# Optimization experiments

Hardware: AMD Instinct MI355X
Metric: run time of the kernel (lower is better)

## Reference

```python
import jax, jax.numpy as jnp
import numpy as np

N = 8192      # batch*seq_len (batch=4, seq_len=2048)
DK = 256
DV = 256


def setup_inputs() -> dict:
    key = jax.random.key(0)
    ks = jax.random.split(key, 9)
    s = 1.0 / np.sqrt(DK)
    return {
        "q": jax.random.normal(ks[0], (N, DK), jnp.float32),
        "k": jax.random.normal(ks[1], (N, DK), jnp.float32),
        "v": jax.random.normal(ks[2], (N, DV), jnp.float32),
        "Wq": jax.random.normal(ks[3], (DK, DK), jnp.float32) * s,
        "bq": jnp.zeros((DK,), jnp.float32),
        "Wk": jax.random.normal(ks[4], (DK, DK), jnp.float32) * s,
        "bk": jnp.zeros((DK,), jnp.float32),
        "Wv": jax.random.normal(ks[5], (DV, DV), jnp.float32) * s,
        "bv": jnp.zeros((DV,), jnp.float32),
        "seq_len": 2048,
    }


def reference(q, k, v, Wq, bq, Wk, bk, Wv, bv, seq_len):
    # torch Linear: y = x @ W.T + b
    Q = q @ Wq.T + bq                       # [N, dk]
    K = k @ Wk.T + bk                       # [N, dk]
    V = v @ Wv.T + bv                       # [N, dv]
    sqrt_dk = jnp.sqrt(jnp.asarray(DK, Q.dtype))
    score = (Q @ K.T) / sqrt_dk             # [N, N] — attends over ALL tokens
    # original reshapes to (B, S, N) and softmaxes over dim=-1, which is
    # identical to row-wise softmax on the [N, N] score matrix
    attn = jax.nn.softmax(score, axis=-1)   # [N, N]
    return attn @ V                          # [N, dv]
```

## Files before the change

kernel.cpp:

```cpp
#include <hip/hip_runtime.h>
#include <hip/hip_bf16.h>


typedef __attribute__((ext_vector_type(8))) short short8;
typedef __attribute__((ext_vector_type(4))) short short4v;
typedef __attribute__((ext_vector_type(4))) float f32x4;
typedef __attribute__((ext_vector_type(4))) float float4v;
typedef __attribute__((ext_vector_type(16))) float f32x16;

#define MFMA16 __builtin_amdgcn_mfma_f32_16x16x32_bf16
#define MFMA32 __builtin_amdgcn_mfma_f32_32x32x16_bf16

namespace {
constexpr int kN = 8192;
constexpr int kD = 256;
constexpr int kKVB = 32;
}

__device__ __forceinline__ unsigned short f2bf(float x) {
  union { float f; unsigned u; } v; v.f = x;
  unsigned r = v.u + 0x7FFFu + ((v.u >> 16) & 1u);
  return (unsigned short)(r >> 16);
}

__device__ __forceinline__ unsigned cvtpk_bf16(float lo, float hi) {
  unsigned d;
  asm("v_cvt_pk_bf16_f32 %0, %1, %2" : "=v"(d) : "v"(lo), "v"(hi));
  return d;
}

__device__ __forceinline__ void plswap(unsigned& a, unsigned& b) {
  auto r = __builtin_amdgcn_permlane32_swap(a, b, false, false);
  a = r[0]; b = r[1];
}
__device__ __forceinline__ float xhalf_sum(float x) {
  unsigned u = __builtin_bit_cast(unsigned, x), v = u;
  plswap(u, v);
  return __builtin_bit_cast(float, u) + __builtin_bit_cast(float, v);
}

__device__ __forceinline__ void gll16(const short* g, const short* lp) {
  __builtin_amdgcn_global_load_lds(
      (const __attribute__((address_space(1))) void*)g,
      (__attribute__((address_space(3))) void*)lp, 16, 0, 0);
}

__device__ __forceinline__ void softmax_pack(f32x16& sacc, short8& pa0, short8& pa1,
                                             float& lsum) {
  float psum = 0.f;
#pragma unroll
  for (int r = 0; r < 16; ++r) { sacc[r] = __expf(sacc[r]); psum += sacc[r]; }
  {
    unsigned A0 = cvtpk_bf16(sacc[0], sacc[1]);
    unsigned A1 = cvtpk_bf16(sacc[2], sacc[3]);
    unsigned B0 = cvtpk_bf16(sacc[4], sacc[5]);
    unsigned B1 = cvtpk_bf16(sacc[6], sacc[7]);
    plswap(A0, B0);
    plswap(A1, B1);
    union { unsigned u[4]; short8 s8; } pu;
    pu.u[0] = A0; pu.u[1] = A1; pu.u[2] = B0; pu.u[3] = B1;
    pa0 = pu.s8;
  }
  {
    unsigned A0 = cvtpk_bf16(sacc[8], sacc[9]);
    unsigned A1 = cvtpk_bf16(sacc[10], sacc[11]);
    unsigned B0 = cvtpk_bf16(sacc[12], sacc[13]);
    unsigned B1 = cvtpk_bf16(sacc[14], sacc[15]);
    plswap(A0, B0);
    plswap(A1, B1);
    union { unsigned u[4]; short8 s8; } pu;
    pu.u[0] = A0; pu.u[1] = A1; pu.u[2] = B0; pu.u[3] = B1;
    pa1 = pu.s8;
  }
  lsum += xhalf_sum(psum);
}

__global__ __launch_bounds__(256, 2) void proj_kernel(
    const float* __restrict__ qx, const float* __restrict__ kx, const float* __restrict__ vx,
    const float* __restrict__ Wq, const float* __restrict__ bq,
    const float* __restrict__ Wk, const float* __restrict__ bk,
    const float* __restrict__ Wv, const float* __restrict__ bv,
    short* __restrict__ Qimg, short* __restrict__ Kimg, short* __restrict__ Vimg)
{
  const int mode = blockIdx.y;
  const float* X; const float* W; const float* B;
  if (mode == 0)      { X = qx; W = Wq; B = bq; }
  else if (mode == 1) { X = kx; W = Wk; B = bk; }
  else                { X = vx; W = Wv; B = bv; }

  const int nb = blockIdx.x * 64;

  __shared__ short XA[64][264];
  __shared__ short WB[64][264];

  const int t  = threadIdx.x;
  const int c4 = t & 63;
  const int r0 = t >> 6;

#pragma unroll
  for (int p = 0; p < 16; ++p) {
    const int r = p * 4 + r0;
    float4v xv = *(const float4v*)(X + (size_t)(nb + r) * kD + c4 * 4);
    short4v xs;
#pragma unroll
    for (int j = 0; j < 4; ++j) xs[j] = (short)f2bf(xv[j]);
    *(short4v*)(&XA[r][c4 * 4]) = xs;
  }

  float4v wreg[16];
#pragma unroll
  for (int p = 0; p < 16; ++p)
    wreg[p] = *(const float4v*)(W + (size_t)(p * 4 + r0) * kD + c4 * 4);

  const int w  = t >> 6;
  const int l  = t & 63;
  const int lr = l & 15;
  const int g  = l >> 4;

  for (int obi = 0; obi < 4; ++obi) {
    __syncthreads();
#pragma unroll
    for (int p = 0; p < 16; ++p) {
      short4v wsv;
#pragma unroll
      for (int j = 0; j < 4; ++j) wsv[j] = (short)f2bf(wreg[p][j]);
      *(short4v*)(&WB[p * 4 + r0][c4 * 4]) = wsv;
    }
    __syncthreads();
    if (obi < 3) {
#pragma unroll
      for (int p = 0; p < 16; ++p)
        wreg[p] = *(const float4v*)(W + (size_t)((obi + 1) * 64 + p * 4 + r0) * kD + c4 * 4);
    }

    const f32x4 vzero = {0.f, 0.f, 0.f, 0.f};
    f32x4 acc[4];
#pragma unroll
    for (int ct = 0; ct < 4; ++ct) acc[ct] = vzero;

    if (mode == 2) {
#pragma unroll
      for (int s = 0; s < 8; ++s) {
        short8 af = *(const short8*)(&XA[w * 16 + lr][s * 32 + g * 8]);
#pragma unroll
        for (int ct = 0; ct < 4; ++ct) {
          short8 bf = *(const short8*)(&WB[ct * 16 + lr][s * 32 + g * 8]);
          acc[ct] = MFMA16(af, bf, acc[ct], 0, 0, 0);
        }
      }
#pragma unroll
      for (int ct = 0; ct < 4; ++ct) {
        const int o = obi * 64 + ct * 16 + lr;
        const float bias = B[o];
        const int n0 = nb + w * 16 + g * 4;
        short4v vs;
#pragma unroll
        for (int r2 = 0; r2 < 4; ++r2) vs[r2] = (short)f2bf(acc[ct][r2] + bias);
        const size_t idx = (size_t)(n0 >> 5) * 8192 + (size_t)(o >> 5) * 1024
                         + (size_t)((n0 >> 4) & 1) * 512 + (size_t)((n0 >> 3) & 1) * 256
                         + (size_t)(o & 31) * 8 + (n0 & 7);
        *(short4v*)(Vimg + idx) = vs;
      }
    } else {
#pragma unroll
      for (int s = 0; s < 8; ++s) {
        short8 af = *(const short8*)(&WB[w * 16 + lr][s * 32 + g * 8]);
#pragma unroll
        for (int ct = 0; ct < 4; ++ct) {
          short8 bf = *(const short8*)(&XA[ct * 16 + lr][s * 32 + g * 8]);
          acc[ct] = MFMA16(af, bf, acc[ct], 0, 0, 0);
        }
      }
      short* Out = (mode == 0) ? Qimg : Kimg;
      const float sc = (mode == 0) ? 0.0625f : 1.0f;
      const int o0 = obi * 64 + w * 16 + g * 4;
      const float4v bv4 = *(const float4v*)(B + o0);
#pragma unroll
      for (int ct = 0; ct < 4; ++ct) {
        const int n = nb + ct * 16 + lr;
        short4v os;
#pragma unroll
        for (int r2 = 0; r2 < 4; ++r2) os[r2] = (short)f2bf((acc[ct][r2] + bv4[r2]) * sc);
        const size_t idx = (size_t)(n >> 5) * 8192 + (size_t)(o0 >> 4) * 512
                         + (size_t)((o0 >> 3) & 1) * 256 + (size_t)(n & 31) * 8 + (o0 & 7);
        *(short4v*)(Out + idx) = os;
      }
    }
  }
}

template<int SPLIT>
__global__ __launch_bounds__(512, 2) void flash_kernel(
    const short* __restrict__ Qimg, const short* __restrict__ Kimg, const short* __restrict__ Vimg,
    short* __restrict__ Ops, float* __restrict__ Ls)
{
  constexpr int kIters = (kN / SPLIT) / kKVB;
  const int linear = (int)blockIdx.x;
  int sp, qb;
  if (SPLIT == 8) { sp = linear & 7; qb = linear >> 3; }
  else { const int xcd = linear & 7; sp = xcd >> 1; qb = ((linear >> 3) << 1) | (xcd & 1); }
  const int kvblk0 = sp * (kN / SPLIT / 32);

  __shared__ short sbuf[3 * 16384];

  const int t = threadIdx.x;
  const int w = t >> 6, l = t & 63;
  const int hf = l >> 5;
  const int lc = l & 31;

  {
    const short* kg = Kimg + (size_t)kvblk0 * 8192 + w * 512 + l * 8;
    const short* vg = Vimg + (size_t)kvblk0 * 8192 + w * 512 + l * 8;
    gll16(kg,        sbuf + w * 512);
    gll16(kg + 4096, sbuf + 4096 + w * 512);
    gll16(vg,        sbuf + 8192 + w * 512);
    gll16(vg + 4096, sbuf + 12288 + w * 512);
  }

  short8 qf[16];
  {
    const short* qsrc = Qimg + (size_t)(qb * 8 + w) * 8192 + l * 8;
#pragma unroll
    for (int ks = 0; ks < 16; ++ks) qf[ks] = *(const short8*)(qsrc + ks * 512);
  }

  f32x16 oacc[8];
#pragma unroll
  for (int dvt = 0; dvt < 8; ++dvt)
#pragma unroll
    for (int r = 0; r < 16; ++r) oacc[dvt][r] = 0.f;
  float lsum = 0.f;
  short8 pa0, pa1;

  asm volatile("s_waitcnt vmcnt(0)" ::: "memory");
  __syncthreads();

  int o_prv = 32768, o_cur = 0, o_nxt = 16384;

  {
    const short* kg = Kimg + (size_t)(kvblk0 + 1) * 8192 + w * 512 + l * 8;
    const short* vg = Vimg + (size_t)(kvblk0 + 1) * 8192 + w * 512 + l * 8;
    gll16(kg,        sbuf + o_nxt + w * 512);
    gll16(kg + 4096, sbuf + o_nxt + 4096 + w * 512);
    gll16(vg,        sbuf + o_nxt + 8192 + w * 512);
    gll16(vg + 4096, sbuf + o_nxt + 12288 + w * 512);

    f32x16 sacc;
#pragma unroll
    for (int r = 0; r < 16; ++r) sacc[r] = 0.f;
    __builtin_amdgcn_s_setprio(1);
#pragma unroll
    for (int ks = 0; ks < 16; ++ks) {
      short8 kf = *(const short8*)(sbuf + o_cur + ks * 512 + l * 8);
      sacc = MFMA32(kf, qf[ks], sacc, 0, 0, 0);
    }
    __builtin_amdgcn_s_setprio(0);
    softmax_pack(sacc, pa0, pa1, lsum);
    __syncthreads();
    int tmp = o_prv; o_prv = o_cur; o_cur = o_nxt; o_nxt = tmp;
  }

  for (int it = 1; it < kIters; ++it) {
    if (it + 1 < kIters) {
      const short* kg = Kimg + (size_t)(kvblk0 + it + 1) * 8192 + w * 512 + l * 8;
      const short* vg = Vimg + (size_t)(kvblk0 + it + 1) * 8192 + w * 512 + l * 8;
      gll16(kg,        sbuf + o_nxt + w * 512);
      gll16(kg + 4096, sbuf + o_nxt + 4096 + w * 512);
      gll16(vg,        sbuf + o_nxt + 8192 + w * 512);
      gll16(vg + 4096, sbuf + o_nxt + 12288 + w * 512);
    }

    f32x16 sacc;
#pragma unroll
    for (int r = 0; r < 16; ++r) sacc[r] = 0.f;
    __builtin_amdgcn_s_setprio(1);
#pragma unroll
    for (int ks = 0; ks < 16; ++ks) {
      short8 kf = *(const short8*)(sbuf + o_cur + ks * 512 + l * 8);
      sacc = MFMA32(kf, qf[ks], sacc, 0, 0, 0);
      short8 vf = *(const short8*)(sbuf + o_prv + 8192 + ks * 512 + l * 8);
      oacc[ks >> 1] = MFMA32((ks & 1) ? pa1 : pa0, vf, oacc[ks >> 1], 0, 0, 0);
    }
    __builtin_amdgcn_s_setprio(0);

    softmax_pack(sacc, pa0, pa1, lsum);
    __syncthreads();
    int tmp = o_prv; o_prv = o_cur; o_cur = o_nxt; o_nxt = tmp;
  }

  __builtin_amdgcn_s_setprio(1);
#pragma unroll
  for (int ks = 0; ks < 16; ++ks) {
    short8 vf = *(const short8*)(sbuf + o_prv + 8192 + ks * 512 + l * 8);
    oacc[ks >> 1] = MFMA32((ks & 1) ? pa1 : pa0, vf, oacc[ks >> 1], 0, 0, 0);
  }
  __builtin_amdgcn_s_setprio(0);

  const float rl = 1.0f / lsum;
  float cs[16];
#pragma unroll
  for (int r = 0; r < 16; ++r)
    cs[r] = __shfl(rl, (r & 3) + 8 * (r >> 2) + 4 * hf) * 4096.f;
  const int qrow0 = qb * 256 + w * 32;
#pragma unroll
  for (int dvt = 0; dvt < 8; ++dvt)
#pragma unroll
    for (int r = 0; r < 16; ++r) {
      const int q = qrow0 + (r & 3) + 8 * (r >> 2) + 4 * hf;
      float x = oacc[dvt][r] * cs[r];
      x = fminf(fmaxf(x, -32767.f), 32767.f);
      Ops[((size_t)sp * kN + q) * kD + dvt * 32 + lc] = (short)(int)rintf(x);
    }
  if (l < 32) Ls[(size_t)sp * kN + qrow0 + l] = lsum;
}

template<int SPLIT>
__global__ __launch_bounds__(256) void merge_kernel(
    const short* __restrict__ Ops, const float* __restrict__ Ls, float* __restrict__ out)
{
  const int t = threadIdx.x;
  const int qrow = blockIdx.x * 8 + (t >> 5);
  const int d0 = (t & 31) * 8;
  float li[SPLIT];
  float denom = 0.f;
#pragma unroll
  for (int s = 0; s < SPLIT; ++s) { li[s] = Ls[(size_t)s * kN + qrow]; denom += li[s]; }
  float n[8];
#pragma unroll
  for (int j = 0; j < 8; ++j) n[j] = 0.f;
#pragma unroll
  for (int s = 0; s < SPLIT; ++s) {
    const short8 u = *(const short8*)(Ops + ((size_t)s * kN + qrow) * kD + d0);
#pragma unroll
    for (int j = 0; j < 8; ++j) n[j] += li[s] * (float)u[j];
  }
  const float inv = 1.0f / (denom * 4096.f);
  float4v o0, o1;
#pragma unroll
  for (int j = 0; j < 4; ++j) { o0[j] = n[j] * inv; o1[j] = n[4 + j] * inv; }
  *(float4v*)(out + (size_t)qrow * kD + d0)     = o0;
  *(float4v*)(out + (size_t)qrow * kD + d0 + 4) = o1;
}

extern "C" void kernel_launch(void* const* d_in, const int* in_sizes, int n_in,
                              void* d_out, int out_size, void* d_ws, size_t ws_size,
                              hipStream_t stream)
{
  const float* q  = (const float*)d_in[0];
  const float* k  = (const float*)d_in[1];
  const float* v  = (const float*)d_in[2];
  const float* Wq = (const float*)d_in[3];
  const float* bq = (const float*)d_in[4];
  const float* Wk = (const float*)d_in[5];
  const float* bk = (const float*)d_in[6];
  const float* Wv = (const float*)d_in[7];
  const float* bv = (const float*)d_in[8];

  char* ws = (char*)d_ws;
  short* Qimg = (short*)(ws);
  short* Kimg = (short*)(ws + ((size_t)4 << 20));
  short* Vimg = (short*)(ws + ((size_t)8 << 20));
  const size_t opOff = (size_t)12 << 20;
  short* Ops = (short*)(ws + opOff);

  proj_kernel<<<dim3(kN / 64, 3), 256, 0, stream>>>(
      q, k, v, Wq, bq, Wk, bk, Wv, bv, Qimg, Kimg, Vimg);

  const size_t opBytes8 = (size_t)8 * kN * kD * 2;
  const size_t need8 = opOff + opBytes8 + (size_t)8 * kN * 4;
  if (ws_size >= need8) {
    float* Ls = (float*)(ws + opOff + opBytes8);
    flash_kernel<8><<<dim3(256), 512, 0, stream>>>(Qimg, Kimg, Vimg, Ops, Ls);
    merge_kernel<8><<<dim3(kN / 8), 256, 0, stream>>>(Ops, Ls, (float*)d_out);
  } else {
    const size_t opBytes4 = (size_t)4 * kN * kD * 2;
    float* Ls = (float*)(ws + opOff + opBytes4);
    flash_kernel<4><<<dim3(128), 512, 0, stream>>>(Qimg, Kimg, Vimg, Ops, Ls);
    merge_kernel<4><<<dim3(kN / 8), 256, 0, stream>>>(Ops, Ls, (float*)d_out);
  }
}
```

Baseline: 97.23 us.

## Process KV tiles in pairs per barrier and fold log2e into Q scale

The flash loop now handles two KV tiles per barrier, staging the next pair of K tiles into a 4-slot ring and V tiles into a 5-slot ring. This halves the number of __syncthreads and vmcnt waits and gives the loads more time in flight, at the cost of more LDS (9×8192 shorts), which may limit occupancy. Separately, log2(e) is folded into the Q projection scale so the softmax can use the raw exp2 instruction instead of __expf, removing a multiply per element.

```diff
diff --git a/kernel.cpp b/kernel.cpp
--- a/kernel.cpp
+++ b/kernel.cpp
@@ -49,7 +49,10 @@
                                              float& lsum) {
   float psum = 0.f;
 #pragma unroll
-  for (int r = 0; r < 16; ++r) { sacc[r] = __expf(sacc[r]); psum += sacc[r]; }
+  for (int r = 0; r < 16; ++r) {
+    sacc[r] = __builtin_amdgcn_exp2f(sacc[r]);
+    psum += sacc[r];
+  }
   {
     unsigned A0 = cvtpk_bf16(sacc[0], sacc[1]);
     unsigned A1 = cvtpk_bf16(sacc[2], sacc[3]);
@@ -172,7 +175,7 @@
         }
       }
       short* Out = (mode == 0) ? Qimg : Kimg;
-      const float sc = (mode == 0) ? 0.0625f : 1.0f;
+      const float sc = (mode == 0) ? (0.0625f * 1.44269504089f) : 1.0f;
       const int o0 = obi * 64 + w * 16 + g * 4;
       const float4v bv4 = *(const float4v*)(B + o0);
 #pragma unroll
@@ -194,28 +197,36 @@
     const short* __restrict__ Qimg, const short* __restrict__ Kimg, const short* __restrict__ Vimg,
     short* __restrict__ Ops, float* __restrict__ Ls)
 {
-  constexpr int kIters = (kN / SPLIT) / kKVB;
+  constexpr int kTiles = (kN / SPLIT) / kKVB;
+  constexpr int kPairs = kTiles / 2;
   const int linear = (int)blockIdx.x;
   int sp, qb;
   if (SPLIT == 8) { sp = linear & 7; qb = linear >> 3; }
   else { const int xcd = linear & 7; sp = xcd >> 1; qb = ((linear >> 3) << 1) | (xcd & 1); }
-  const int kvblk0 = sp * (kN / SPLIT / 32);
-
-  __shared__ short sbuf[3 * 16384];
+  const int kvblk0 = sp * kTiles;
+
+  __shared__ short sbuf[4 * 8192 + 5 * 8192];
 
   const int t = threadIdx.x;
   const int w = t >> 6, l = t & 63;
   const int hf = l >> 5;
   const int lc = l & 31;
 
-  {
-    const short* kg = Kimg + (size_t)kvblk0 * 8192 + w * 512 + l * 8;
-    const short* vg = Vimg + (size_t)kvblk0 * 8192 + w * 512 + l * 8;
-    gll16(kg,        sbuf + w * 512);
-    gll16(kg + 4096, sbuf + 4096 + w * 512);
-    gll16(vg,        sbuf + 8192 + w * 512);
-    gll16(vg + 4096, sbuf + 12288 + w * 512);
-  }
+  auto stageK = [&](int tile, int slot) {
+    const short* kg = Kimg + (size_t)(kvblk0 + tile) * 8192 + w * 512 + l * 8;
+    const short* d = sbuf + slot * 8192 + w * 512;
+    gll16(kg, d);
+    gll16(kg + 4096, d + 4096);
+  };
+  auto stageV = [&](int tile, int slot) {
+    const short* vg = Vimg + (size_t)(kvblk0 + tile) * 8192 + w * 512 + l * 8;
+    const short* d = sbuf + 32768 + slot * 8192 + w * 512;
+    gll16(vg, d);
+    gll16(vg + 4096, d + 4096);
+  };
+
+  stageK(0, 0); stageV(0, 0);
+  stageK(1, 1); stageV(1, 1);
 
   short8 qf[16];
   {
@@ -235,66 +246,86 @@
   asm volatile("s_waitcnt vmcnt(0)" ::: "memory");
   __syncthreads();
 
-  int o_prv = 32768, o_cur = 0, o_nxt = 16384;
+  auto qk_pv = [&](int kslot, int vslot, f32x16& sacc) {
+    const short* kb = sbuf + kslot * 8192 + l * 8;
+    const short* vb = sbuf + 32768 + vslot * 8192 + l * 8;
+    __builtin_amdgcn_s_setprio(1);
+#pragma unroll
+    for (int ks = 0; ks < 16; ++ks) {
+      short8 kf = *(const short8*)(kb + ks * 512);
+      sacc = MFMA32(kf, qf[ks], sacc, 0, 0, 0);
+      short8 vf = *(const short8*)(vb + ks * 512);
+      oacc[ks >> 1] = MFMA32((ks & 1) ? pa1 : pa0, vf, oacc[ks >> 1], 0, 0, 0);
+    }
+    __builtin_amdgcn_s_setprio(0);
+  };
 
   {
-    const short* kg = Kimg + (size_t)(kvblk0 + 1) * 8192 + w * 512 + l * 8;
-    const short* vg = Vimg + (size_t)(kvblk0 + 1) * 8192 + w * 512 + l * 8;
-    gll16(kg,        sbuf + o_nxt + w * 512);
-    gll16(kg + 4096, sbuf + o_nxt + 4096 + w * 512);
-    gll16(vg,        sbuf + o_nxt + 8192 + w * 512);
-    gll16(vg + 4096, sbuf + o_nxt + 12288 + w * 512);
-
+    if (kPairs > 1) { stageK(2, 2); stageV(2, 2); stageK(3, 3); stageV(3, 3); }
     f32x16 sacc;
 #pragma unroll
     for (int r = 0; r < 16; ++r) sacc[r] = 0.f;
+    const short* kb = sbuf + l * 8;
     __builtin_amdgcn_s_setprio(1);
 #pragma unroll
     for (int ks = 0; ks < 16; ++ks) {
-      short8 kf = *(const short8*)(sbuf + o_cur + ks * 512 + l * 8);
+      short8 kf = *(const short8*)(kb + ks * 512);
       sacc = MFMA32(kf, qf[ks], sacc, 0, 0, 0);
     }
     __builtin_amdgcn_s_setprio(0);
     softmax_pack(sacc, pa0, pa1, lsum);
+
+    f32x16 sacc1;
+#pragma unroll
+    for (int r = 0; r < 16; ++r) sacc1[r] = 0.f;
+    qk_pv(1, 0, sacc1);
+    softmax_pack(sacc1, pa0, pa1, lsum);
+
+    asm volatile("s_waitcnt vmcnt(0)" ::: "memory");
     __syncthreads();
-    int tmp = o_prv; o_prv = o_cur; o_cur = o_nxt; o_nxt = tmp;
-  }
-
-  for (int it = 1; it < kIters; ++it) {
-    if (it + 1 < kIters) {
-      const short* kg = Kimg + (size_t)(kvblk0 + it + 1) * 8192 + w * 512 + l * 8;
-      const short* vg = Vimg + (size_t)(kvblk0 + it + 1) * 8192 + w * 512 + l * 8;
-      gll16(kg,        sbuf + o_nxt + w * 512);
-      gll16(kg + 4096, sbuf + o_nxt + 4096 + w * 512);
-      gll16(vg,        sbuf + o_nxt + 8192 + w * 512);
-      gll16(vg + 4096, sbuf + o_nxt + 12288 + w * 512);
+  }
+
+  int v_m1 = 1;
+  for (int tt = 1; tt < kPairs; ++tt) {
+    const int a = 2 * tt;
+    const int v0 = (v_m1 == 4) ? 0 : v_m1 + 1;
+    const int v1 = (v0 == 4) ? 0 : v0 + 1;
+    if (tt + 1 < kPairs) {
+      const int v2 = (v1 == 4) ? 0 : v1 + 1;
+      const int v3 = (v2 == 4) ? 0 : v2 + 1;
+      stageK(a + 2, (a + 2) & 3); stageV(a + 2, v2);
+      stageK(a + 3, (a + 3) & 3); stageV(a + 3, v3);
     }
 
     f32x16 sacc;
 #pragma unroll
     for (int r = 0; r < 16; ++r) sacc[r] = 0.f;
+    qk_pv(a & 3, v_m1, sacc);
+    softmax_pack(sacc, pa0, pa1, lsum);
+
+    f32x16 sacc1;
+#pragma unroll
+    for (int r = 0; r < 16; ++r) sacc1[r] = 0.f;
+    qk_pv((a + 1) & 3, v0, sacc1);
+    softmax_pack(sacc1, pa0, pa1, lsum);
+
+    if (tt + 1 < kPairs) {
+      asm volatile("s_waitcnt vmcnt(0)" ::: "memory");
+      __syncthreads();
+    }
+    v_m1 = v1;
+  }
+
+  {
+    const short* vb = sbuf + 32768 + v_m1 * 8192 + l * 8;
     __builtin_amdgcn_s_setprio(1);
 #pragma unroll
     for (int ks = 0; ks < 16; ++ks) {
-      short8 kf = *(const short8*)(sbuf + o_cur + ks * 512 + l * 8);
-      sacc = MFMA32(kf, qf[ks], sacc, 0, 0, 0);
-      short8 vf = *(const short8*)(sbuf + o_prv + 8192 + ks * 512 + l * 8);
+      short8 vf = *(const short8*)(vb + ks * 512);
       oacc[ks >> 1] = MFMA32((ks & 1) ? pa1 : pa0, vf, oacc[ks >> 1], 0, 0, 0);
     }
     __builtin_amdgcn_s_setprio(0);
-
-    softmax_pack(sacc, pa0, pa1, lsum);
-    __syncthreads();
-    int tmp = o_prv; o_prv = o_cur; o_cur = o_nxt; o_nxt = tmp;
-  }
-
-  __builtin_amdgcn_s_setprio(1);
-#pragma unroll
-  for (int ks = 0; ks < 16; ++ks) {
-    short8 vf = *(const short8*)(sbuf + o_prv + 8192 + ks * 512 + l * 8);
-    oacc[ks >> 1] = MFMA32((ks & 1) ? pa1 : pa0, vf, oacc[ks >> 1], 0, 0, 0);
-  }
-  __builtin_amdgcn_s_setprio(0);
+  }
 
   const float rl = 1.0f / lsum;
   float cs[16];
```

After: 97.14 us. About the same (-0.1%).
